# Kernel tuning notes

Hardware: AMD Instinct MI355X
Metric: run time of the kernel (lower is better)

Reference implementation:

```python
import jax, jax.numpy as jnp
import numpy as np

N, NQ, M, DQ, DK, DV, H = 4, 512, 512, 256, 256, 256, 256


def setup_inputs() -> dict:
    key = jax.random.key(0)
    ks = jax.random.split(key, 6)
    scale_q = 1.0 / np.sqrt(DQ)
    scale_k = 1.0 / np.sqrt(DK)
    scale_v = 1.0 / np.sqrt(H)
    return {
        "query": jax.random.normal(ks[0], (N, NQ, DQ), jnp.float32),
        "key": jax.random.normal(ks[1], (N, M, DK), jnp.float32),
        "value": jax.random.normal(ks[2], (N, M, DV), jnp.float32),
        "W_q": jax.random.normal(ks[3], (DQ, H), jnp.float32) * scale_q,
        "W_k": jax.random.normal(ks[4], (DK, H), jnp.float32) * scale_k,
        "W_v": jax.random.normal(ks[5], (H,), jnp.float32) * scale_v,
    }


def reference(query, key, value, W_q, W_k, W_v):
    # project: (N, n, H) and (N, m, H)
    q = jnp.einsum("bnd,dh->bnh", query, W_q)
    k = jnp.einsum("bmd,dh->bmh", key, W_k)
    # broadcast add -> (N, n, m, H), tanh, project H->1 -> scores (N, n, m)
    scores = jnp.einsum("bnmh,h->bnm", jnp.tanh(q[:, :, None, :] + k[:, None, :, :]), W_v)
    attn = jax.nn.softmax(scores, axis=-1)  # (N, n, m)
    return jnp.einsum("bnm,bmv->bnv", attn, value)
```

## Files before the change

### kernel.cpp

```cpp
#include <hip/hip_runtime.h>

#define NB 4
#define NQL 512
#define ML 512
#define DDIM 256
#define HDIM 256

static constexpr float TWO_LOG2E = 2.8853900817779268f;
static constexpr float LOG2E     = 1.4426950408889634f;

#define SB() __builtin_amdgcn_sched_barrier(0)

#define PJC(xs0, xs1, wv)                              \
    acc[0][0] = fmaf(xs0, (wv).x, acc[0][0]);          \
    acc[0][1] = fmaf(xs0, (wv).y, acc[0][1]);          \
    acc[0][2] = fmaf(xs0, (wv).z, acc[0][2]);          \
    acc[0][3] = fmaf(xs0, (wv).w, acc[0][3]);          \
    acc[1][0] = fmaf(xs1, (wv).x, acc[1][0]);          \
    acc[1][1] = fmaf(xs1, (wv).y, acc[1][1]);          \
    acc[1][2] = fmaf(xs1, (wv).z, acc[1][2]);          \
    acc[1][3] = fmaf(xs1, (wv).w, acc[1][3]);

#define PJ_LOAD(X0, X1, Wr, c)                                         \
    {                                                                  \
        const int d0_ = (c) * 8;                                       \
        X0[0] = *(const float4*)(xr0 + d0_);                           \
        X0[1] = *(const float4*)(xr0 + d0_ + 4);                       \
        X1[0] = *(const float4*)(xr1 + d0_);                           \
        X1[1] = *(const float4*)(xr1 + d0_ + 4);                       \
        _Pragma("unroll")                                              \
        for (int r_ = 0; r_ < 8; ++r_)                                 \
            Wr[r_] = *(const float4*)(wc + (size_t)(d0_ + r_) * HDIM); \
    }

#define PJ_COMP(X0, X1, Wr)                        \
    PJC(X0[0].x, X1[0].x, Wr[0])                   \
    PJC(X0[0].y, X1[0].y, Wr[1])                   \
    PJC(X0[0].z, X1[0].z, Wr[2])                   \
    PJC(X0[0].w, X1[0].w, Wr[3])                   \
    PJC(X0[1].x, X1[1].x, Wr[4])                   \
    PJC(X0[1].y, X1[1].y, Wr[5])                   \
    PJC(X0[1].z, X1[1].z, Wr[6])                   \
    PJC(X0[1].w, X1[1].w, Wr[7])

__global__ __launch_bounds__(512) void proj_kernel(
    const float* __restrict__ q_src, const float* __restrict__ k_src,
    const float* __restrict__ Wq,    const float* __restrict__ Wk,
    float* __restrict__ EqT,         float* __restrict__ EkT)
{
    const int idx   = blockIdx.x;
    const int b     = idx & 3;
    const int which = (idx >> 2) & 1;
    const int lt    = (idx >> 3) & 7;
    const int ht    = idx >> 6;
    const float* __restrict__ src = which ? k_src : q_src;
    const float* __restrict__ W   = which ? Wk : Wq;
    float* __restrict__ outT      = which ? EkT : EqT;

    const int l0 = lt * 64, h0 = ht * 64;
    const int t  = threadIdx.x;
    const int tx = t & 15;
    const int ty = t >> 4;

    const float* xr0 = &src[(size_t)(b * NQL + l0 + ty * 2) * DDIM];
    const float* xr1 = xr0 + DDIM;
    const float* wc  = &W[h0 + tx * 4];

    float4 XA0[2], XA1[2], WA[8];
    float4 XB0[2], XB1[2], WB[8];
    float acc[2][4] = {};

    PJ_LOAD(XA0, XA1, WA, 0)
    SB();
    for (int v = 0; v < 15; ++v) {
        PJ_LOAD(XB0, XB1, WB, 2 * v + 1)
        SB();
        PJ_COMP(XA0, XA1, WA)
        SB();
        PJ_LOAD(XA0, XA1, WA, 2 * v + 2)
        SB();
        PJ_COMP(XB0, XB1, WB)
        SB();
    }
    PJ_LOAD(XB0, XB1, WB, 31)
    SB();
    PJ_COMP(XA0, XA1, WA)
    SB();
    PJ_COMP(XB0, XB1, WB)

    #pragma unroll
    for (int j = 0; j < 4; ++j) {
        float2 o;
        o.x = __builtin_amdgcn_exp2f(acc[0][j] * TWO_LOG2E);
        o.y = __builtin_amdgcn_exp2f(acc[1][j] * TWO_LOG2E);
        *(float2*)&outT[(size_t)(b * HDIM + h0 + tx * 4 + j) * NQL + l0 + ty * 2] = o;
    }
}

#define SC_EVAL(Q, K, j, wv)                                 \
    {                                                        \
        swv += (wv);                                         \
        const float nw2 = -2.0f * (wv);                      \
        float a00 = fmaf(Q[j].x, K[j].x, 1.0f);              \
        float a01 = fmaf(Q[j].x, K[j].y, 1.0f);              \
        float a02 = fmaf(Q[j].x, K[j].z, 1.0f);              \
        float a03 = fmaf(Q[j].x, K[j].w, 1.0f);              \
        float a10 = fmaf(Q[j].y, K[j].x, 1.0f);              \
        float a11 = fmaf(Q[j].y, K[j].y, 1.0f);              \
        float a12 = fmaf(Q[j].y, K[j].z, 1.0f);              \
        float a13 = fmaf(Q[j].y, K[j].w, 1.0f);              \
        float r0 = __builtin_amdgcn_rcpf(a00 * a01);         \
        float r1 = __builtin_amdgcn_rcpf(a02 * a03);         \
        float r2 = __builtin_amdgcn_rcpf(a10 * a11);         \
        float r3 = __builtin_amdgcn_rcpf(a12 * a13);         \
        float t0 = nw2 * r0, t1 = nw2 * r1;                  \
        float t2 = nw2 * r2, t3 = nw2 * r3;                  \
        acc0[0] = fmaf(t0, a01, acc0[0]);                    \
        acc0[1] = fmaf(t0, a00, acc0[1]);                    \
        acc0[2] = fmaf(t1, a03, acc0[2]);                    \
        acc0[3] = fmaf(t1, a02, acc0[3]);                    \
        acc1[0] = fmaf(t2, a11, acc1[0]);                    \
        acc1[1] = fmaf(t2, a10, acc1[1]);                    \
        acc1[2] = fmaf(t3, a13, acc1[2]);                    \
        acc1[3] = fmaf(t3, a12, acc1[3]);                    \
    }

#define SC_LOAD(Q, K, Wb, c)                                           \
    {                                                                  \
        const int h0_ = (c) * 4;                                       \
        _Pragma("unroll")                                              \
        for (int j_ = 0; j_ < 4; ++j_) {                               \
            Q[j_]  = *(const float2*)(qbase + (size_t)(h0_ + j_) * NQL); \
            K[j_]  = *(const float4*)(kbase + (size_t)(h0_ + j_) * ML);  \
            Wb[j_] = Wv[h0_ + j_];                                     \
        }                                                              \
    }

#define SC_COMP(Q, K, Wb)                                              \
    { SC_EVAL(Q, K, 0, Wb[0]) SC_EVAL(Q, K, 1, Wb[1])                  \
      SC_EVAL(Q, K, 2, Wb[2]) SC_EVAL(Q, K, 3, Wb[3]) }

__global__ __launch_bounds__(512) void scores_kernel(
    const float* __restrict__ EqT, const float* __restrict__ EkT,
    const float* __restrict__ Wv, float* __restrict__ P,
    float* __restrict__ Spart)
{
    const int idx = blockIdx.x;
    const int b   = idx & 3;
    const int mt  = (idx >> 2) & 3;
    const int nt  = idx >> 4;
    const int m0  = mt * 128, n0 = nt * 32;
    const int t   = threadIdx.x;
    const int tx  = t & 31;
    const int ty  = t >> 5;

    const float* qbase = &EqT[(size_t)b * HDIM * NQL + n0 + ty * 2];
    const float* kbase = &EkT[(size_t)b * HDIM * ML + m0 + tx * 4];

    float2 QA[4], QB[4];
    float4 KA[4], KB[4];
    float  WA[4], WB[4];
    float acc0[4] = {}, acc1[4] = {};
    float swv = 0.f;

    SC_LOAD(QA, KA, WA, 0)
    SB();
    for (int v = 0; v < 31; ++v) {
        SC_LOAD(QB, KB, WB, 2 * v + 1)
        SB();
        SC_COMP(QA, KA, WA)
        SB();
        SC_LOAD(QA, KA, WA, 2 * v + 2)
        SB();
        SC_COMP(QB, KB, WB)
        SB();
    }
    SC_LOAD(QB, KB, WB, 63)
    SB();
    SC_COMP(QA, KA, WA)
    SB();
    SC_COMP(QB, KB, WB)

    float rs[2];
    {
        float4 p;
        p.x = __builtin_amdgcn_exp2f((swv + acc0[0]) * LOG2E);
        p.y = __builtin_amdgcn_exp2f((swv + acc0[1]) * LOG2E);
        p.z = __builtin_amdgcn_exp2f((swv + acc0[2]) * LOG2E);
        p.w = __builtin_amdgcn_exp2f((swv + acc0[3]) * LOG2E);
        *(float4*)&P[(size_t)(b * NQL + n0 + ty * 2 + 0) * ML + m0 + tx * 4] = p;
        rs[0] = (p.x + p.y) + (p.z + p.w);
    }
    {
        float4 p;
        p.x = __builtin_amdgcn_exp2f((swv + acc1[0]) * LOG2E);
        p.y = __builtin_amdgcn_exp2f((swv + acc1[1]) * LOG2E);
        p.z = __builtin_amdgcn_exp2f((swv + acc1[2]) * LOG2E);
        p.w = __builtin_amdgcn_exp2f((swv + acc1[3]) * LOG2E);
        *(float4*)&P[(size_t)(b * NQL + n0 + ty * 2 + 1) * ML + m0 + tx * 4] = p;
        rs[1] = (p.x + p.y) + (p.z + p.w);
    }
    #pragma unroll
    for (int off = 1; off < 32; off <<= 1) {
        rs[0] += __shfl_xor(rs[0], off);
        rs[1] += __shfl_xor(rs[1], off);
    }
    if (tx == 0) {
        float2 o = {rs[0], rs[1]};
        *(float2*)&Spart[(size_t)(mt * NB + b) * NQL + n0 + ty * 2] = o;
    }
}

#define AV_ONE(PSb, VSb, i, r, comp)                                 \
    acc[i][0] = fmaf(PSb[i].comp, VSb[r].x, acc[i][0]);              \
    acc[i][1] = fmaf(PSb[i].comp, VSb[r].y, acc[i][1]);              \
    acc[i][2] = fmaf(PSb[i].comp, VSb[r].z, acc[i][2]);              \
    acc[i][3] = fmaf(PSb[i].comp, VSb[r].w, acc[i][3]);
#define AV_RR(PSb, VSb, r, comp)                                     \
    AV_ONE(PSb, VSb, 0, r, comp) AV_ONE(PSb, VSb, 1, r, comp)        \
    AV_ONE(PSb, VSb, 2, r, comp) AV_ONE(PSb, VSb, 3, r, comp)
#define AV_COMP(PSb, VSb)                                            \
    AV_RR(PSb, VSb, 0, x) AV_RR(PSb, VSb, 1, y)                      \
    AV_RR(PSb, VSb, 2, z) AV_RR(PSb, VSb, 3, w)

#define AV_LOAD(PSb, VSb, c)                                              \
    {                                                                     \
        const int mm_ = (c) * 4;                                          \
        _Pragma("unroll")                                                 \
        for (int r_ = 0; r_ < 4; ++r_) {                                  \
            PSb[r_] = *(const float4*)(pbase + (size_t)r_ * ML + mm_);    \
            VSb[r_] = *(const float4*)(vbase + (size_t)(mm_ + r_) * DDIM);\
        }                                                                 \
    }

__global__ __launch_bounds__(256) void av_kernel(
    const float* __restrict__ P, const float* __restrict__ Spart,
    const float* __restrict__ V, float* __restrict__ O)
{
    const int idx = blockIdx.x;
    const int b   = idx & 3;
    const int vt  = (idx >> 2) & 3;
    const int nt  = idx >> 4;
    const int v0  = vt * 64, n0 = nt * 16;
    const int t    = threadIdx.x;
    const int lane = t & 63;
    const int wid  = t >> 6;
    const int tx   = lane & 15;
    const int tn   = lane >> 4;

    __shared__ float sInv[16];
    __shared__ float sRed[3][16][64];

    if (t < 16) {
        float s = 0.f;
        #pragma unroll
        for (int mt = 0; mt < 4; ++mt)
            s += Spart[(size_t)(mt * NB + b) * NQL + n0 + t];
        sInv[t] = 1.0f / s;
    }

    const float* pbase = &P[(size_t)(b * NQL + n0 + tn * 4) * ML + wid * 128];
    const float* vbase = &V[(size_t)(b * ML + wid * 128) * DDIM + v0 + tx * 4];

    float4 PA[4], VA[4];
    float4 PB[4], VB[4];
    float acc[4][4] = {};

    AV_LOAD(PA, VA, 0)
    SB();
    for (int v = 0; v < 15; ++v) {
        AV_LOAD(PB, VB, 2 * v + 1)
        SB();
        AV_COMP(PA, VA)
        SB();
        AV_LOAD(PA, VA, 2 * v + 2)
        SB();
        AV_COMP(PB, VB)
        SB();
    }
    AV_LOAD(PB, VB, 31)
    SB();
    AV_COMP(PA, VA)
    SB();
    AV_COMP(PB, VB)

    __syncthreads();
    if (wid != 0) {
        #pragma unroll
        for (int i = 0; i < 4; ++i) {
            float4 r = {acc[i][0], acc[i][1], acc[i][2], acc[i][3]};
            *(float4*)&sRed[wid - 1][tn * 4 + i][tx * 4] = r;
        }
    }
    __syncthreads();
    if (wid == 0) {
        #pragma unroll
        for (int i = 0; i < 4; ++i) {
            float4 r1 = *(const float4*)&sRed[0][tn * 4 + i][tx * 4];
            float4 r2 = *(const float4*)&sRed[1][tn * 4 + i][tx * 4];
            float4 r3 = *(const float4*)&sRed[2][tn * 4 + i][tx * 4];
            const float inv = sInv[tn * 4 + i];
            float4 o;
            o.x = (acc[i][0] + r1.x + r2.x + r3.x) * inv;
            o.y = (acc[i][1] + r1.y + r2.y + r3.y) * inv;
            o.z = (acc[i][2] + r1.z + r2.z + r3.z) * inv;
            o.w = (acc[i][3] + r1.w + r2.w + r3.w) * inv;
            *(float4*)&O[(size_t)(b * NQL + n0 + tn * 4 + i) * DDIM + v0 + tx * 4] = o;
        }
    }
}

extern "C" void kernel_launch(void* const* d_in, const int* in_sizes, int n_in,
                              void* d_out, int out_size, void* d_ws, size_t ws_size,
                              hipStream_t stream)
{
    const float* query = (const float*)d_in[0];
    const float* key   = (const float*)d_in[1];
    const float* value = (const float*)d_in[2];
    const float* Wq    = (const float*)d_in[3];
    const float* Wk    = (const float*)d_in[4];
    const float* Wv    = (const float*)d_in[5];
    float* out = (float*)d_out;

    float* EqT   = (float*)d_ws;
    float* EkT   = EqT + (size_t)NB * HDIM * NQL;
    float* P     = EkT + (size_t)NB * HDIM * ML;
    float* Spart = P + (size_t)NB * NQL * ML;

    proj_kernel<<<dim3(256), 512, 0, stream>>>(query, key, Wq, Wk, EqT, EkT);
    scores_kernel<<<dim3(256), 512, 0, stream>>>(EqT, EkT, Wv, P, Spart);
    av_kernel<<<dim3(512), 256, 0, stream>>>(P, Spart, value, out);
}
```

Measured before the change: 143.6 us.

## Tile scores kernel through double-buffered LDS and enlarge projection register tile

The scores kernel now stages 32-row chunks of the transposed Q and K projections in double-buffered shared memory, and each thread computes a 4x2 output tile. It uses 512 blocks of 256 threads with 16 partial row-sum slices, and the AV kernel sums all 16. The projection kernel switches to 256 threads with 4x4 register tiles. This aims to cut redundant global loads and raise arithmetic intensity, at the cost of barriers, LDS traffic, and more partial sums.

```diff
diff --git a/kernel.cpp b/kernel.cpp
--- a/kernel.cpp
+++ b/kernel.cpp
@@ -11,39 +11,34 @@
 
 #define SB() __builtin_amdgcn_sched_barrier(0)
 
-#define PJC(xs0, xs1, wv)                              \
-    acc[0][0] = fmaf(xs0, (wv).x, acc[0][0]);          \
-    acc[0][1] = fmaf(xs0, (wv).y, acc[0][1]);          \
-    acc[0][2] = fmaf(xs0, (wv).z, acc[0][2]);          \
-    acc[0][3] = fmaf(xs0, (wv).w, acc[0][3]);          \
-    acc[1][0] = fmaf(xs1, (wv).x, acc[1][0]);          \
-    acc[1][1] = fmaf(xs1, (wv).y, acc[1][1]);          \
-    acc[1][2] = fmaf(xs1, (wv).z, acc[1][2]);          \
-    acc[1][3] = fmaf(xs1, (wv).w, acc[1][3]);
-
-#define PJ_LOAD(X0, X1, Wr, c)                                         \
-    {                                                                  \
-        const int d0_ = (c) * 8;                                       \
-        X0[0] = *(const float4*)(xr0 + d0_);                           \
-        X0[1] = *(const float4*)(xr0 + d0_ + 4);                       \
-        X1[0] = *(const float4*)(xr1 + d0_);                           \
-        X1[1] = *(const float4*)(xr1 + d0_ + 4);                       \
-        _Pragma("unroll")                                              \
-        for (int r_ = 0; r_ < 8; ++r_)                                 \
-            Wr[r_] = *(const float4*)(wc + (size_t)(d0_ + r_) * HDIM); \
-    }
-
-#define PJ_COMP(X0, X1, Wr)                        \
-    PJC(X0[0].x, X1[0].x, Wr[0])                   \
-    PJC(X0[0].y, X1[0].y, Wr[1])                   \
-    PJC(X0[0].z, X1[0].z, Wr[2])                   \
-    PJC(X0[0].w, X1[0].w, Wr[3])                   \
-    PJC(X0[1].x, X1[1].x, Wr[4])                   \
-    PJC(X0[1].y, X1[1].y, Wr[5])                   \
-    PJC(X0[1].z, X1[1].z, Wr[6])                   \
-    PJC(X0[1].w, X1[1].w, Wr[7])
-
-__global__ __launch_bounds__(512) void proj_kernel(
+#define PJ_LOAD(Xr, Wr, c)                                          \
+    {                                                               \
+        const int d_ = (c) * 4;                                     \
+        Xr[0] = *(const float4*)(xr0 + d_);                         \
+        Xr[1] = *(const float4*)(xr1 + d_);                         \
+        Xr[2] = *(const float4*)(xr2 + d_);                         \
+        Xr[3] = *(const float4*)(xr3 + d_);                         \
+        Wr[0] = *(const float4*)(wc + (size_t)(d_ + 0) * HDIM);     \
+        Wr[1] = *(const float4*)(wc + (size_t)(d_ + 1) * HDIM);     \
+        Wr[2] = *(const float4*)(wc + (size_t)(d_ + 2) * HDIM);     \
+        Wr[3] = *(const float4*)(wc + (size_t)(d_ + 3) * HDIM);     \
+    }
+
+#define PJ_FMA(Xr, Wr, i, comp, r)                                  \
+    acc[i][0] = fmaf(Xr[i].comp, Wr[r].x, acc[i][0]);               \
+    acc[i][1] = fmaf(Xr[i].comp, Wr[r].y, acc[i][1]);               \
+    acc[i][2] = fmaf(Xr[i].comp, Wr[r].z, acc[i][2]);               \
+    acc[i][3] = fmaf(Xr[i].comp, Wr[r].w, acc[i][3]);
+
+#define PJ_ROW(Xr, Wr, i)                                           \
+    PJ_FMA(Xr, Wr, i, x, 0) PJ_FMA(Xr, Wr, i, y, 1)                 \
+    PJ_FMA(Xr, Wr, i, z, 2) PJ_FMA(Xr, Wr, i, w, 3)
+
+#define PJ_COMP(Xr, Wr)                                             \
+    PJ_ROW(Xr, Wr, 0) PJ_ROW(Xr, Wr, 1)                             \
+    PJ_ROW(Xr, Wr, 2) PJ_ROW(Xr, Wr, 3)
+
+__global__ __launch_bounds__(256) void proj_kernel(
     const float* __restrict__ q_src, const float* __restrict__ k_src,
     const float* __restrict__ Wq,    const float* __restrict__ Wk,
     float* __restrict__ EqT,         float* __restrict__ EkT)
@@ -62,152 +57,142 @@
     const int tx = t & 15;
     const int ty = t >> 4;
 
-    const float* xr0 = &src[(size_t)(b * NQL + l0 + ty * 2) * DDIM];
+    const float* xr0 = &src[(size_t)(b * NQL + l0 + ty * 4) * DDIM];
     const float* xr1 = xr0 + DDIM;
+    const float* xr2 = xr0 + 2 * DDIM;
+    const float* xr3 = xr0 + 3 * DDIM;
     const float* wc  = &W[h0 + tx * 4];
 
-    float4 XA0[2], XA1[2], WA[8];
-    float4 XB0[2], XB1[2], WB[8];
-    float acc[2][4] = {};
-
-    PJ_LOAD(XA0, XA1, WA, 0)
-    SB();
-    for (int v = 0; v < 15; ++v) {
-        PJ_LOAD(XB0, XB1, WB, 2 * v + 1)
-        SB();
-        PJ_COMP(XA0, XA1, WA)
-        SB();
-        PJ_LOAD(XA0, XA1, WA, 2 * v + 2)
-        SB();
-        PJ_COMP(XB0, XB1, WB)
-        SB();
-    }
-    PJ_LOAD(XB0, XB1, WB, 31)
-    SB();
-    PJ_COMP(XA0, XA1, WA)
-    SB();
-    PJ_COMP(XB0, XB1, WB)
+    float4 XA[4], WA[4], XB[4], WB[4];
+    float acc[4][4] = {};
+
+    PJ_LOAD(XA, WA, 0)
+    SB();
+    for (int v = 0; v < 31; ++v) {
+        PJ_LOAD(XB, WB, 2 * v + 1)
+        SB();
+        PJ_COMP(XA, WA)
+        SB();
+        PJ_LOAD(XA, WA, 2 * v + 2)
+        SB();
+        PJ_COMP(XB, WB)
+        SB();
+    }
+    PJ_LOAD(XB, WB, 63)
+    SB();
+    PJ_COMP(XA, WA)
+    SB();
+    PJ_COMP(XB, WB)
 
     #pragma unroll
     for (int j = 0; j < 4; ++j) {
-        float2 o;
+        float4 o;
         o.x = __builtin_amdgcn_exp2f(acc[0][j] * TWO_LOG2E);
         o.y = __builtin_amdgcn_exp2f(acc[1][j] * TWO_LOG2E);
-        *(float2*)&outT[(size_t)(b * HDIM + h0 + tx * 4 + j) * NQL + l0 + ty * 2] = o;
+        o.z = __builtin_amdgcn_exp2f(acc[2][j] * TWO_LOG2E);
+        o.w = __builtin_amdgcn_exp2f(acc[3][j] * TWO_LOG2E);
+        *(float4*)&outT[(size_t)(b * HDIM + h0 + tx * 4 + j) * NQL + l0 + ty * 4] = o;
     }
 }
 
-#define SC_EVAL(Q, K, j, wv)                                 \
-    {                                                        \
-        swv += (wv);                                         \
-        const float nw2 = -2.0f * (wv);                      \
-        float a00 = fmaf(Q[j].x, K[j].x, 1.0f);              \
-        float a01 = fmaf(Q[j].x, K[j].y, 1.0f);              \
-        float a02 = fmaf(Q[j].x, K[j].z, 1.0f);              \
-        float a03 = fmaf(Q[j].x, K[j].w, 1.0f);              \
-        float a10 = fmaf(Q[j].y, K[j].x, 1.0f);              \
-        float a11 = fmaf(Q[j].y, K[j].y, 1.0f);              \
-        float a12 = fmaf(Q[j].y, K[j].z, 1.0f);              \
-        float a13 = fmaf(Q[j].y, K[j].w, 1.0f);              \
-        float r0 = __builtin_amdgcn_rcpf(a00 * a01);         \
-        float r1 = __builtin_amdgcn_rcpf(a02 * a03);         \
-        float r2 = __builtin_amdgcn_rcpf(a10 * a11);         \
-        float r3 = __builtin_amdgcn_rcpf(a12 * a13);         \
-        float t0 = nw2 * r0, t1 = nw2 * r1;                  \
-        float t2 = nw2 * r2, t3 = nw2 * r3;                  \
-        acc0[0] = fmaf(t0, a01, acc0[0]);                    \
-        acc0[1] = fmaf(t0, a00, acc0[1]);                    \
-        acc0[2] = fmaf(t1, a03, acc0[2]);                    \
-        acc0[3] = fmaf(t1, a02, acc0[3]);                    \
-        acc1[0] = fmaf(t2, a11, acc1[0]);                    \
-        acc1[1] = fmaf(t2, a10, acc1[1]);                    \
-        acc1[2] = fmaf(t3, a13, acc1[2]);                    \
-        acc1[3] = fmaf(t3, a12, acc1[3]);                    \
-    }
-
-#define SC_LOAD(Q, K, Wb, c)                                           \
-    {                                                                  \
-        const int h0_ = (c) * 4;                                       \
-        _Pragma("unroll")                                              \
-        for (int j_ = 0; j_ < 4; ++j_) {                               \
-            Q[j_]  = *(const float2*)(qbase + (size_t)(h0_ + j_) * NQL); \
-            K[j_]  = *(const float4*)(kbase + (size_t)(h0_ + j_) * ML);  \
-            Wb[j_] = Wv[h0_ + j_];                                     \
-        }                                                              \
-    }
-
-#define SC_COMP(Q, K, Wb)                                              \
-    { SC_EVAL(Q, K, 0, Wb[0]) SC_EVAL(Q, K, 1, Wb[1])                  \
-      SC_EVAL(Q, K, 2, Wb[2]) SC_EVAL(Q, K, 3, Wb[3]) }
-
-__global__ __launch_bounds__(512) void scores_kernel(
+__global__ __launch_bounds__(256) void scores_kernel(
     const float* __restrict__ EqT, const float* __restrict__ EkT,
     const float* __restrict__ Wv, float* __restrict__ P,
     float* __restrict__ Spart)
 {
     const int idx = blockIdx.x;
     const int b   = idx & 3;
-    const int mt  = (idx >> 2) & 3;
-    const int nt  = idx >> 4;
-    const int m0  = mt * 128, n0 = nt * 32;
+    const int mt  = (idx >> 2) & 15;
+    const int nt  = idx >> 6;
+    const int m0  = mt * 32, n0 = nt * 64;
     const int t   = threadIdx.x;
-    const int tx  = t & 31;
-    const int ty  = t >> 5;
-
-    const float* qbase = &EqT[(size_t)b * HDIM * NQL + n0 + ty * 2];
-    const float* kbase = &EkT[(size_t)b * HDIM * ML + m0 + tx * 4];
-
-    float2 QA[4], QB[4];
-    float4 KA[4], KB[4];
-    float  WA[4], WB[4];
-    float acc0[4] = {}, acc1[4] = {};
+    const int tx  = t & 15;
+    const int ty  = t >> 4;
+
+    __shared__ float sQ[2][32][68];
+    __shared__ float sK[2][32][36];
+
+    const int rq = t >> 3, cq = t & 7;
+    const int rk = t >> 3, ck = t & 7;
+
+    const float* qbase = &EqT[(size_t)b * HDIM * NQL + n0];
+    const float* kbase = &EkT[(size_t)b * HDIM * ML + m0];
+
+    float4 q1 = *(const float4*)(qbase + (size_t)rq * NQL + cq * 8);
+    float4 q2 = *(const float4*)(qbase + (size_t)rq * NQL + cq * 8 + 4);
+    float4 kv = *(const float4*)(kbase + (size_t)rk * ML + ck * 4);
+
+    float acc[4][2] = {};
     float swv = 0.f;
-
-    SC_LOAD(QA, KA, WA, 0)
-    SB();
-    for (int v = 0; v < 31; ++v) {
-        SC_LOAD(QB, KB, WB, 2 * v + 1)
-        SB();
-        SC_COMP(QA, KA, WA)
-        SB();
-        SC_LOAD(QA, KA, WA, 2 * v + 2)
-        SB();
-        SC_COMP(QB, KB, WB)
-        SB();
-    }
-    SC_LOAD(QB, KB, WB, 63)
-    SB();
-    SC_COMP(QA, KA, WA)
-    SB();
-    SC_COMP(QB, KB, WB)
-
-    float rs[2];
-    {
-        float4 p;
-        p.x = __builtin_amdgcn_exp2f((swv + acc0[0]) * LOG2E);
-        p.y = __builtin_amdgcn_exp2f((swv + acc0[1]) * LOG2E);
-        p.z = __builtin_amdgcn_exp2f((swv + acc0[2]) * LOG2E);
-        p.w = __builtin_amdgcn_exp2f((swv + acc0[3]) * LOG2E);
-        *(float4*)&P[(size_t)(b * NQL + n0 + ty * 2 + 0) * ML + m0 + tx * 4] = p;
-        rs[0] = (p.x + p.y) + (p.z + p.w);
-    }
-    {
-        float4 p;
-        p.x = __builtin_amdgcn_exp2f((swv + acc1[0]) * LOG2E);
-        p.y = __builtin_amdgcn_exp2f((swv + acc1[1]) * LOG2E);
-        p.z = __builtin_amdgcn_exp2f((swv + acc1[2]) * LOG2E);
-        p.w = __builtin_amdgcn_exp2f((swv + acc1[3]) * LOG2E);
-        *(float4*)&P[(size_t)(b * NQL + n0 + ty * 2 + 1) * ML + m0 + tx * 4] = p;
-        rs[1] = (p.x + p.y) + (p.z + p.w);
-    }
+    int cur = 0;
+
+    for (int c = 0; c < 8; ++c) {
+        *(float4*)&sQ[cur][rq][cq * 8]     = q1;
+        *(float4*)&sQ[cur][rq][cq * 8 + 4] = q2;
+        *(float4*)&sK[cur][rk][ck * 4]     = kv;
+        __syncthreads();
+        if (c < 7) {
+            const float* qn = qbase + (size_t)((c + 1) * 32 + rq) * NQL;
+            q1 = *(const float4*)(qn + cq * 8);
+            q2 = *(const float4*)(qn + cq * 8 + 4);
+            kv = *(const float4*)(kbase + (size_t)((c + 1) * 32 + rk) * ML + ck * 4);
+        }
+        const float* wvp = Wv + c * 32;
+        #pragma unroll 8
+        for (int hh = 0; hh < 32; ++hh) {
+            float4 q4 = *(const float4*)&sQ[cur][hh][ty * 4];
+            float2 k2 = *(const float2*)&sK[cur][hh][tx * 2];
+            const float wv = wvp[hh];
+            swv += wv;
+            const float nw2 = -2.0f * wv;
+            {
+                float a0 = fmaf(q4.x, k2.x, 1.0f);
+                float a1 = fmaf(q4.y, k2.x, 1.0f);
+                float a2 = fmaf(q4.z, k2.x, 1.0f);
+                float a3 = fmaf(q4.w, k2.x, 1.0f);
+                float r01 = __builtin_amdgcn_rcpf(a0 * a1);
+                float r23 = __builtin_amdgcn_rcpf(a2 * a3);
+                float t01 = nw2 * r01, t23 = nw2 * r23;
+                acc[0][0] = fmaf(t01, a1, acc[0][0]);
+                acc[1][0] = fmaf(t01, a0, acc[1][0]);
+                acc[2][0] = fmaf(t23, a3, acc[2][0]);
+                acc[3][0] = fmaf(t23, a2, acc[3][0]);
+            }
+            {
+                float a0 = fmaf(q4.x, k2.y, 1.0f);
+                float a1 = fmaf(q4.y, k2.y, 1.0f);
+                float a2 = fmaf(q4.z, k2.y, 1.0f);
+                float a3 = fmaf(q4.w, k2.y, 1.0f);
+                float r01 = __builtin_amdgcn_rcpf(a0 * a1);
+                float r23 = __builtin_amdgcn_rcpf(a2 * a3);
+                float t01 = nw2 * r01, t23 = nw2 * r23;
+                acc[0][1] = fmaf(t01, a1, acc[0][1]);
+                acc[1][1] = fmaf(t01, a0, acc[1][1]);
+                acc[2][1] = fmaf(t23, a3, acc[2][1]);
+                acc[3][1] = fmaf(t23, a2, acc[3][1]);
+            }
+        }
+        cur ^= 1;
+    }
+
+    float rs[4];
     #pragma unroll
-    for (int off = 1; off < 32; off <<= 1) {
-        rs[0] += __shfl_xor(rs[0], off);
-        rs[1] += __shfl_xor(rs[1], off);
+    for (int i = 0; i < 4; ++i) {
+        float2 p;
+        p.x = __builtin_amdgcn_exp2f((swv + acc[i][0]) * LOG2E);
+        p.y = __builtin_amdgcn_exp2f((swv + acc[i][1]) * LOG2E);
+        *(float2*)&P[(size_t)(b * NQL + n0 + ty * 4 + i) * ML + m0 + tx * 2] = p;
+        rs[i] = p.x + p.y;
+    }
+    #pragma unroll
+    for (int off = 1; off < 16; off <<= 1) {
+        #pragma unroll
+        for (int i = 0; i < 4; ++i) rs[i] += __shfl_xor(rs[i], off);
     }
     if (tx == 0) {
-        float2 o = {rs[0], rs[1]};
-        *(float2*)&Spart[(size_t)(mt * NB + b) * NQL + n0 + ty * 2] = o;
+        #pragma unroll
+        for (int i = 0; i < 4; ++i)
+            Spart[(size_t)(mt * NB + b) * NQL + n0 + ty * 4 + i] = rs[i];
     }
 }
 
@@ -254,7 +239,7 @@
     if (t < 16) {
         float s = 0.f;
         #pragma unroll
-        for (int mt = 0; mt < 4; ++mt)
+        for (int mt = 0; mt < 16; ++mt)
             s += Spart[(size_t)(mt * NB + b) * NQL + n0 + t];
         sInv[t] = 1.0f / s;
     }
@@ -327,7 +312,7 @@
     float* P     = EkT + (size_t)NB * HDIM * ML;
     float* Spart = P + (size_t)NB * NQL * ML;
 
-    proj_kernel<<<dim3(256), 512, 0, stream>>>(query, key, Wq, Wk, EqT, EkT);
-    scores_kernel<<<dim3(256), 512, 0, stream>>>(EqT, EkT, Wv, P, Spart);
+    proj_kernel<<<dim3(256), 256, 0, stream>>>(query, key, Wq, Wk, EqT, EkT);
+    scores_kernel<<<dim3(512), 256, 0, stream>>>(EqT, EkT, Wv, P, Spart);
     av_kernel<<<dim3(512), 256, 0, stream>>>(P, Spart, value, out);
 }
```

Result: no change. 142.9 us (-0.4%).
